# Optimization experiments

Measured on AMD Instinct MI355X. Metric: run time of the kernel, lower is better.

## Reference

```python
import jax, jax.numpy as jnp
import numpy as np

NC = 80
REG_MAX = 16
NO = REG_MAX * 4 + NC  # 144
LEVEL_SHAPES = [(80, 80), (40, 40), (20, 20)]
STRIDES = [8.0, 16.0, 32.0]
CHANNELS = [256, 512, 512]


def _make_anchors():
    """Returns anchor_points (2, A) and stride_tensor (1, A), grid offset 0.5."""
    pts, sts = [], []
    for (h, w), s in zip(LEVEL_SHAPES, STRIDES):
        sx = jnp.arange(w, dtype=jnp.float32) + 0.5
        sy = jnp.arange(h, dtype=jnp.float32) + 0.5
        gy, gx = jnp.meshgrid(sy, sx, indexing='ij')
        pts.append(jnp.stack([gx.ravel(), gy.ravel()], axis=-1))  # (h*w, 2)
        sts.append(jnp.full((h * w,), s, dtype=jnp.float32))
    anchors = jnp.concatenate(pts, axis=0).T          # (2, A)
    strides = jnp.concatenate(sts, axis=0)[None, :]   # (1, A)
    return anchors, strides


def setup_inputs() -> dict:
    key = jax.random.key(0)
    ks = jax.random.split(key, 16)
    inp = {}
    inp['x0'] = jax.random.normal(ks[0], (16, 256, 80, 80), dtype=jnp.float32)
    inp['x1'] = jax.random.normal(ks[1], (16, 512, 40, 40), dtype=jnp.float32)
    inp['x2'] = jax.random.normal(ks[2], (16, 512, 20, 20), dtype=jnp.float32)
    # per-level 1x1 conv head weights: box branch (4*reg_max out), cls branch (nc out)
    for i, c in enumerate(CHANNELS):
        sc = 1.0 / np.sqrt(c)
        inp[f'w_box{i}'] = jax.random.normal(ks[3 + 4 * i], (REG_MAX * 4, c), dtype=jnp.float32) * sc
        inp[f'b_box{i}'] = jax.random.normal(ks[4 + 4 * i], (REG_MAX * 4,), dtype=jnp.float32) * 0.01
        inp[f'w_cls{i}'] = jax.random.normal(ks[5 + 4 * i], (NC, c), dtype=jnp.float32) * sc
        inp[f'b_cls{i}'] = jax.random.normal(ks[6 + 4 * i], (NC,), dtype=jnp.float32) * 0.01
    return inp


def _level_out(x, wb, bb, wc, bc):
    # cat(cv2(x), cv3(x), dim=1) then view(B, no, -1)
    box = jnp.einsum('bchw,oc->bohw', x, wb) + bb[None, :, None, None]
    cls = jnp.einsum('bchw,oc->bohw', x, wc) + bc[None, :, None, None]
    B = x.shape[0]
    return jnp.concatenate([box, cls], axis=1).reshape(B, NO, -1)


def reference(x0, x1, x2,
              w_box0, b_box0, w_cls0, b_cls0,
              w_box1, b_box1, w_cls1, b_cls1,
              w_box2, b_box2, w_cls2, b_cls2):
    xs = [x0, x1, x2]
    wbs = [w_box0, w_box1, w_box2]
    bbs = [b_box0, b_box1, b_box2]
    wcs = [w_cls0, w_cls1, w_cls2]
    bcs = [b_cls0, b_cls1, b_cls2]
    x_cat = jnp.concatenate(
        [_level_out(x, wb, bb, wc, bc) for x, wb, bb, wc, bc in zip(xs, wbs, bbs, wcs, bcs)],
        axis=2)  # (B, 144, A)
    B, _, A = x_cat.shape
    box, cls = x_cat[:, :REG_MAX * 4, :], x_cat[:, REG_MAX * 4:, :]

    # DFL: (B, 4*16, A) -> softmax over 16 bins -> expected distance per side
    p = jax.nn.softmax(box.reshape(B, 4, REG_MAX, A), axis=2)
    dist = jnp.einsum('bkra,r->bka', p, jnp.arange(REG_MAX, dtype=jnp.float32))  # (B, 4, A)

    # dist2bbox (xywh) on anchor grid, scale by stride
    anchors, strides = _make_anchors()
    anc = anchors[None]                 # (1, 2, A)
    lt, rb = dist[:, :2, :], dist[:, 2:, :]
    x1y1 = anc - lt
    x2y2 = anc + rb
    c_xy = (x1y1 + x2y2) * 0.5
    wh = x2y2 - x1y1
    dbox = jnp.concatenate([c_xy, wh], axis=1) * strides[:, None, :]  # (B, 4, A)

    # boxes (B, A, 4), scores (B, A, nc) -- the tensors fed to EfficientNMS_TRT
    boxes = jnp.transpose(dbox, (0, 2, 1))
    scores = jnp.transpose(cls, (0, 2, 1))
    return jnp.concatenate([boxes, scores], axis=-1)  # (B, A, 4 + nc)
```

## Files before the change

kernel.cpp:

```cpp
#include <hip/hip_runtime.h>


typedef __bf16 bf16x8 __attribute__((ext_vector_type(8)));
typedef float  f32x4  __attribute__((ext_vector_type(4)));

#define NTHREADS 256

#define WCHUNK 9216
#define WOFF0 0
#define WOFF1 73728
#define WOFF2 221184

#define XBUF 16384

__device__ __forceinline__ unsigned int pack_bf16(float a, float b) {
    unsigned int ua = __builtin_bit_cast(unsigned int, a);
    unsigned int ub = __builtin_bit_cast(unsigned int, b);
    return ((ua + 0x8000u) >> 16) | ((ub + 0x8000u) & 0xffff0000u);
}

__device__ __forceinline__ int swz32(int row, int kbyte) {
    return row * 64 + (kbyte ^ ((((row & 3) ^ ((row >> 2) & 1))) << 4));
}

__device__ __forceinline__ void gload_lds16(const void* g, void* l) {
    __builtin_amdgcn_global_load_lds(
        (const __attribute__((address_space(1))) void*)g,
        (__attribute__((address_space(3))) void*)l, 16, 0, 0);
}

__global__ __launch_bounds__(256)
void prep_w_kernel(const float* __restrict__ wb0, const float* __restrict__ wc0,
                   const float* __restrict__ wb1, const float* __restrict__ wc1,
                   const float* __restrict__ wb2, const float* __restrict__ wc2,
                   unsigned char* __restrict__ ws) {
    int uid = blockIdx.x * 256 + threadIdx.x;
    if (uid >= 23040) return;
    const float* wb; const float* wc; int C; size_t off; int uu;
    if (uid < 4608)       { wb = wb0; wc = wc0; C = 256; off = WOFF0; uu = uid; }
    else if (uid < 13824) { wb = wb1; wc = wc1; C = 512; off = WOFF1; uu = uid - 4608; }
    else                  { wb = wb2; wc = wc2; C = 512; off = WOFF2; uu = uid - 13824; }
    const int kunits = C / 8;
    const int row = uu / kunits;
    const int k   = (uu % kunits) * 8;
    const float* src = ((row < 64) ? (wb + row * C) : (wc + (row - 64) * C)) + k;
    const float4 f0 = *(const float4*)(src);
    const float4 f1 = *(const float4*)(src + 4);
    uint4 p;
    p.x = pack_bf16(f0.x, f0.y);
    p.y = pack_bf16(f0.z, f0.w);
    p.z = pack_bf16(f1.x, f1.y);
    p.w = pack_bf16(f1.z, f1.w);
    const int chunk = k >> 5;
    const int kg    = (k & 31) >> 3;
    *(uint4*)(ws + off + (size_t)chunk * WCHUNK + swz32(row, kg * 16)) = p;
}

template <int LVL>
__device__ __forceinline__ void run_level(
        int rb,
        const float* __restrict__ x,
        const unsigned char* __restrict__ wimg_all,
        const float* __restrict__ bbox, const float* __restrict__ bcls,
        float* __restrict__ out,
        unsigned char* s_w, unsigned char* s_x) {

    constexpr int    C      = (LVL == 0) ? 256 : 512;
    constexpr int    GW     = (LVL == 0) ? 80 : (LVL == 1 ? 40 : 20);
    constexpr int    HW     = GW * GW;
    constexpr int    AOFF   = (LVL == 0) ? 0 : (LVL == 1 ? 6400 : 8000);
    constexpr float  STRIDE = (LVL == 0) ? 8.0f : (LVL == 1 ? 16.0f : 32.0f);
    constexpr int    TPB    = (HW + 127) / 128;
    constexpr size_t WOFF   = (LVL == 0) ? WOFF0 : (LVL == 1 ? WOFF1 : WOFF2);
    const int nkc = C / 32;

    const int b    = rb / TPB;
    const int tile = rb % TPB;
    int hw0 = tile * 128;
    if (hw0 > HW - 128) hw0 = HW - 128;

    const int tid  = threadIdx.x;
    const int wv   = tid >> 6;
    const int lane = tid & 63;
    const int col  = lane & 15;
    const int q4   = lane >> 4;

    const float* xlev = x + (size_t)b * C * HW;
    const unsigned char* wimg = wimg_all + WOFF;

    const int xg  = (((lane & 31) ^ (wv << 2)) << 2);
    const int xr  = lane >> 5;
    const int xrd0 = (((wv * 32 + col) << 2) ^ (q4 << 6)) + q4 * 8 * 512;
    const int xrd1 = (((wv * 32 + 16 + col) << 2) ^ (q4 << 6)) + q4 * 8 * 512;

    f32x4 acc[9][2];
#pragma unroll
    for (int m = 0; m < 9; ++m) {
        acc[m][0] = (f32x4){0.f, 0.f, 0.f, 0.f};
        acc[m][1] = (f32x4){0.f, 0.f, 0.f, 0.f};
    }

#define XDMA(CC, BUF)                                                       \
    {                                                                       \
        _Pragma("unroll")                                                   \
        for (int _i = 0; _i < 4; ++_i) {                                    \
            const int _r2 = wv * 8 + _i * 2;                                \
            gload_lds16(xlev + (size_t)((CC) * 32 + _r2 + xr) * HW + hw0 + xg, \
                        s_x + (BUF) * XBUF + _r2 * 512);                    \
        }                                                                   \
    }

#define WDMA(CC, BUF)                                                       \
    {                                                                       \
        _Pragma("unroll")                                                   \
        for (int _i = 0; _i < 3; ++_i) {                                    \
            const int _u = tid + _i * 256;                                  \
            if (_u < 576)                                                   \
                gload_lds16(wimg + (size_t)(CC) * WCHUNK + _u * 16,         \
                            s_w + (BUF) * WCHUNK + _u * 16);                \
        }                                                                   \
    }

    XDMA(0, 0);
    WDMA(0, 0);
    __builtin_amdgcn_sched_barrier(0);
    asm volatile("s_waitcnt vmcnt(0)" ::: "memory");
    __builtin_amdgcn_s_barrier();
    __builtin_amdgcn_sched_barrier(0);

    for (int kc = 0; kc < nkc; ++kc) {
        const int cur = kc & 1;
        const bool more = (kc + 1 < nkc);

        if (more) {
            XDMA(kc + 1, cur ^ 1);
            WDMA(kc + 1, cur ^ 1);
        }
        __builtin_amdgcn_sched_barrier(0);

        const unsigned char* xbuf = s_x + cur * XBUF;
        float xf0[8], xf1[8];
#pragma unroll
        for (int j = 0; j < 8; ++j) {
            xf0[j] = *(const float*)(xbuf + xrd0 + j * 512);
            xf1[j] = *(const float*)(xbuf + xrd1 + j * 512);
        }
        uint4 qa, qb;
        qa.x = pack_bf16(xf0[0], xf0[1]); qa.y = pack_bf16(xf0[2], xf0[3]);
        qa.z = pack_bf16(xf0[4], xf0[5]); qa.w = pack_bf16(xf0[6], xf0[7]);
        qb.x = pack_bf16(xf1[0], xf1[1]); qb.y = pack_bf16(xf1[2], xf1[3]);
        qb.z = pack_bf16(xf1[4], xf1[5]); qb.w = pack_bf16(xf1[6], xf1[7]);
        const bf16x8 fA = __builtin_bit_cast(bf16x8, qa);
        const bf16x8 fB = __builtin_bit_cast(bf16x8, qb);

        const unsigned char* wbuf = s_w + cur * WCHUNK;
#pragma unroll
        for (int m = 0; m < 9; ++m) {
            const bf16x8 a_ = *(const bf16x8*)(wbuf + swz32(m * 16 + col, q4 * 16));
            acc[m][0] = __builtin_amdgcn_mfma_f32_16x16x32_bf16(a_, fA, acc[m][0], 0, 0, 0);
            acc[m][1] = __builtin_amdgcn_mfma_f32_16x16x32_bf16(a_, fB, acc[m][1], 0, 0, 0);
        }
        __builtin_amdgcn_sched_barrier(0);

        if (more) {
            asm volatile("s_waitcnt vmcnt(0)" ::: "memory");
            __builtin_amdgcn_s_barrier();
            __builtin_amdgcn_sched_barrier(0);
        }
    }

#undef WDMA
#undef XDMA

    float4 bcv[5];
#pragma unroll
    for (int m = 0; m < 5; ++m)
        bcv[m] = *(const float4*)(bcls + m * 16 + q4 * 4);

    const float LOG2E = 1.44269504088896f;

#pragma unroll
    for (int nf = 0; nf < 2; ++nf) {
        const int alocal = wv * 32 + nf * 16 + col;
        const int hw = hw0 + alocal;

        float dist[4];
#pragma unroll
        for (int g = 0; g < 4; ++g) {
            const float4 bbv = *(const float4*)(bbox + g * 16 + q4 * 4);
            const float v0 = acc[g][nf][0] + bbv.x;
            const float v1 = acc[g][nf][1] + bbv.y;
            const float v2 = acc[g][nf][2] + bbv.z;
            const float v3 = acc[g][nf][3] + bbv.w;
            float mx = fmaxf(fmaxf(v0, v1), fmaxf(v2, v3));
            mx = fmaxf(mx, __shfl_xor(mx, 16));
            mx = fmaxf(mx, __shfl_xor(mx, 32));
            const float e0 = __builtin_amdgcn_exp2f((v0 - mx) * LOG2E);
            const float e1 = __builtin_amdgcn_exp2f((v1 - mx) * LOG2E);
            const float e2 = __builtin_amdgcn_exp2f((v2 - mx) * LOG2E);
            const float e3 = __builtin_amdgcn_exp2f((v3 - mx) * LOG2E);
            float s  = e0 + e1 + e2 + e3;
            float ws = e1 + 2.f * e2 + 3.f * e3 + (float)(q4 * 4) * s;
            s  += __shfl_xor(s, 16);
            s  += __shfl_xor(s, 32);
            ws += __shfl_xor(ws, 16);
            ws += __shfl_xor(ws, 32);
            dist[g] = ws / s;
        }

        const size_t obase = ((size_t)b * 8400 + AOFF + hw) * 84;
        if (q4 == 0) {
            const float ax = (float)(hw % GW) + 0.5f;
            const float ay = (float)(hw / GW) + 0.5f;
            f32x4 bx;
            bx[0] = (ax + 0.5f * (dist[2] - dist[0])) * STRIDE;
            bx[1] = (ay + 0.5f * (dist[3] - dist[1])) * STRIDE;
            bx[2] = (dist[0] + dist[2]) * STRIDE;
            bx[3] = (dist[1] + dist[3]) * STRIDE;
            *(f32x4*)(out + obase) = bx;
        }
#pragma unroll
        for (int m = 0; m < 5; ++m) {
            f32x4 v;
            v[0] = acc[m + 4][nf][0] + bcv[m].x;
            v[1] = acc[m + 4][nf][1] + bcv[m].y;
            v[2] = acc[m + 4][nf][2] + bcv[m].z;
            v[3] = acc[m + 4][nf][3] + bcv[m].w;
            *(f32x4*)(out + obase + 4 + m * 16 + q4 * 4) = v;
        }
    }
}

__global__ __launch_bounds__(NTHREADS, 3)
void UltralyticsDetect_kernel(
        const float* __restrict__ x0, const float* __restrict__ x1, const float* __restrict__ x2,
        const unsigned char* __restrict__ wimg,
        const float* __restrict__ bb0, const float* __restrict__ bc0,
        const float* __restrict__ bb1, const float* __restrict__ bc1,
        const float* __restrict__ bb2, const float* __restrict__ bc2,
        float* __restrict__ out) {

    __shared__ __align__(16) unsigned char s_w[2 * WCHUNK];
    __shared__ __align__(16) unsigned char s_x[2 * XBUF];

    const int bid = blockIdx.x;
    if (bid < 208) {
        run_level<1>(bid, x1, wimg, bb1, bc1, out, s_w, s_x);
    } else if (bid < 272) {
        run_level<2>(bid - 208, x2, wimg, bb2, bc2, out, s_w, s_x);
    } else {
        run_level<0>(bid - 272, x0, wimg, bb0, bc0, out, s_w, s_x);
    }
}

extern "C" void kernel_launch(void* const* d_in, const int* in_sizes, int n_in,
                              void* d_out, int out_size, void* d_ws, size_t ws_size,
                              hipStream_t stream) {
    const float* x0  = (const float*)d_in[0];
    const float* x1  = (const float*)d_in[1];
    const float* x2  = (const float*)d_in[2];
    const float* wb0 = (const float*)d_in[3];
    const float* bb0 = (const float*)d_in[4];
    const float* wc0 = (const float*)d_in[5];
    const float* bc0 = (const float*)d_in[6];
    const float* wb1 = (const float*)d_in[7];
    const float* bb1 = (const float*)d_in[8];
    const float* wc1 = (const float*)d_in[9];
    const float* bc1 = (const float*)d_in[10];
    const float* wb2 = (const float*)d_in[11];
    const float* bb2 = (const float*)d_in[12];
    const float* wc2 = (const float*)d_in[13];
    const float* bc2 = (const float*)d_in[14];

    unsigned char* wimg = (unsigned char*)d_ws;

    prep_w_kernel<<<90, 256, 0, stream>>>(wb0, wc0, wb1, wc1, wb2, wc2, wimg);

    UltralyticsDetect_kernel<<<1072, NTHREADS, 0, stream>>>(
        x0, x1, x2, wimg,
        bb0, bc0, bb1, bc1, bb2, bc2,
        (float*)d_out);
}
```

Measured before the change: 48.30 us.

## Load MFMA weight fragments directly from global memory in lane order, drop LDS weight staging

The weight prep kernel now writes bf16 weights in per-lane MFMA fragment order, so each lane can read its A operand straight from global memory (served from L2/L1) instead of DMA-staging weight chunks into LDS. The weight shared buffer is dropped, which frees LDS and may allow more resident blocks. The per-level template is folded into one kernel with runtime level parameters. The explicit waitcnt and sched barriers are replaced by __syncthreads. The cost is global-load latency on the MFMA operand path inside the inner loop, and weaker scheduling control because the level constants are now runtime values.

```diff
diff --git a/kernel.cpp b/kernel.cpp
--- a/kernel.cpp
+++ b/kernel.cpp
@@ -17,10 +17,6 @@
     unsigned int ua = __builtin_bit_cast(unsigned int, a);
     unsigned int ub = __builtin_bit_cast(unsigned int, b);
     return ((ua + 0x8000u) >> 16) | ((ub + 0x8000u) & 0xffff0000u);
-}
-
-__device__ __forceinline__ int swz32(int row, int kbyte) {
-    return row * 64 + (kbyte ^ ((((row & 3) ^ ((row >> 2) & 1))) << 4));
 }
 
 __device__ __forceinline__ void gload_lds16(const void* g, void* l) {
@@ -51,31 +47,40 @@
     p.y = pack_bf16(f0.z, f0.w);
     p.z = pack_bf16(f1.x, f1.y);
     p.w = pack_bf16(f1.z, f1.w);
-    const int chunk = k >> 5;
-    const int kg    = (k & 31) >> 3;
-    *(uint4*)(ws + off + (size_t)chunk * WCHUNK + swz32(row, kg * 16)) = p;
-}
-
-template <int LVL>
-__device__ __forceinline__ void run_level(
-        int rb,
-        const float* __restrict__ x,
-        const unsigned char* __restrict__ wimg_all,
-        const float* __restrict__ bbox, const float* __restrict__ bcls,
-        float* __restrict__ out,
-        unsigned char* s_w, unsigned char* s_x) {
-
-    constexpr int    C      = (LVL == 0) ? 256 : 512;
-    constexpr int    GW     = (LVL == 0) ? 80 : (LVL == 1 ? 40 : 20);
-    constexpr int    HW     = GW * GW;
-    constexpr int    AOFF   = (LVL == 0) ? 0 : (LVL == 1 ? 6400 : 8000);
-    constexpr float  STRIDE = (LVL == 0) ? 8.0f : (LVL == 1 ? 16.0f : 32.0f);
-    constexpr int    TPB    = (HW + 127) / 128;
-    constexpr size_t WOFF   = (LVL == 0) ? WOFF0 : (LVL == 1 ? WOFF1 : WOFF2);
+    const int kc   = k >> 5;
+    const int m    = row >> 4;
+    const int lane = (row & 15) | (((k & 31) >> 3) << 4);
+    *(uint4*)(ws + off + (size_t)kc * WCHUNK + m * 1024 + lane * 16) = p;
+}
+
+__global__ __launch_bounds__(NTHREADS, 3)
+void UltralyticsDetect_kernel(
+        const float* __restrict__ x0, const float* __restrict__ x1, const float* __restrict__ x2,
+        const unsigned char* __restrict__ wimg,
+        const float* __restrict__ bb0, const float* __restrict__ bc0,
+        const float* __restrict__ bb1, const float* __restrict__ bc1,
+        const float* __restrict__ bb2, const float* __restrict__ bc2,
+        float* __restrict__ out) {
+
+    __shared__ __align__(16) unsigned char s_x[2 * XBUF];
+
+    const int bid = blockIdx.x;
+    const float* x; const float* bbox; const float* bcls;
+    int C, GW, HW, AOFF, TPB, rb; float STRIDE; size_t WOFF;
+    if (bid < 208) {
+        x = x1; bbox = bb1; bcls = bc1; rb = bid;
+        C = 512; GW = 40; HW = 1600; AOFF = 6400; TPB = 13; STRIDE = 16.0f; WOFF = WOFF1;
+    } else if (bid < 272) {
+        x = x2; bbox = bb2; bcls = bc2; rb = bid - 208;
+        C = 512; GW = 20; HW = 400;  AOFF = 8000; TPB = 4;  STRIDE = 32.0f; WOFF = WOFF2;
+    } else {
+        x = x0; bbox = bb0; bcls = bc0; rb = bid - 272;
+        C = 256; GW = 80; HW = 6400; AOFF = 0;    TPB = 50; STRIDE = 8.0f;  WOFF = WOFF0;
+    }
     const int nkc = C / 32;
 
     const int b    = rb / TPB;
-    const int tile = rb % TPB;
+    const int tile = rb - b * TPB;
     int hw0 = tile * 128;
     if (hw0 > HW - 128) hw0 = HW - 128;
 
@@ -86,7 +91,7 @@
     const int q4   = lane >> 4;
 
     const float* xlev = x + (size_t)b * C * HW;
-    const unsigned char* wimg = wimg_all + WOFF;
+    const unsigned char* wlev = wimg + WOFF + (size_t)lane * 16;
 
     const int xg  = (((lane & 31) ^ (wv << 2)) << 2);
     const int xr  = lane >> 5;
@@ -110,35 +115,13 @@
         }                                                                   \
     }
 
-#define WDMA(CC, BUF)                                                       \
-    {                                                                       \
-        _Pragma("unroll")                                                   \
-        for (int _i = 0; _i < 3; ++_i) {                                    \
-            const int _u = tid + _i * 256;                                  \
-            if (_u < 576)                                                   \
-                gload_lds16(wimg + (size_t)(CC) * WCHUNK + _u * 16,         \
-                            s_w + (BUF) * WCHUNK + _u * 16);                \
-        }                                                                   \
-    }
-
     XDMA(0, 0);
-    WDMA(0, 0);
-    __builtin_amdgcn_sched_barrier(0);
-    asm volatile("s_waitcnt vmcnt(0)" ::: "memory");
-    __builtin_amdgcn_s_barrier();
-    __builtin_amdgcn_sched_barrier(0);
+    __syncthreads();
 
     for (int kc = 0; kc < nkc; ++kc) {
-        const int cur = kc & 1;
-        const bool more = (kc + 1 < nkc);
-
-        if (more) {
-            XDMA(kc + 1, cur ^ 1);
-            WDMA(kc + 1, cur ^ 1);
-        }
-        __builtin_amdgcn_sched_barrier(0);
-
-        const unsigned char* xbuf = s_x + cur * XBUF;
+        if (kc + 1 < nkc) XDMA(kc + 1, (kc & 1) ^ 1);
+
+        const unsigned char* xbuf = s_x + (kc & 1) * XBUF;
         float xf0[8], xf1[8];
 #pragma unroll
         for (int j = 0; j < 8; ++j) {
@@ -153,23 +136,17 @@
         const bf16x8 fA = __builtin_bit_cast(bf16x8, qa);
         const bf16x8 fB = __builtin_bit_cast(bf16x8, qb);
 
-        const unsigned char* wbuf = s_w + cur * WCHUNK;
+        const unsigned char* wk = wlev + (size_t)kc * WCHUNK;
 #pragma unroll
         for (int m = 0; m < 9; ++m) {
-            const bf16x8 a_ = *(const bf16x8*)(wbuf + swz32(m * 16 + col, q4 * 16));
+            const bf16x8 a_ = *(const bf16x8*)(wk + m * 1024);
             acc[m][0] = __builtin_amdgcn_mfma_f32_16x16x32_bf16(a_, fA, acc[m][0], 0, 0, 0);
             acc[m][1] = __builtin_amdgcn_mfma_f32_16x16x32_bf16(a_, fB, acc[m][1], 0, 0, 0);
         }
-        __builtin_amdgcn_sched_barrier(0);
-
-        if (more) {
-            asm volatile("s_waitcnt vmcnt(0)" ::: "memory");
-            __builtin_amdgcn_s_barrier();
-            __builtin_amdgcn_sched_barrier(0);
-        }
-    }
-
-#undef WDMA
+
+        __syncthreads();
+    }
+
 #undef XDMA
 
     float4 bcv[5];
@@ -231,28 +208,6 @@
     }
 }
 
-__global__ __launch_bounds__(NTHREADS, 3)
-void UltralyticsDetect_kernel(
-        const float* __restrict__ x0, const float* __restrict__ x1, const float* __restrict__ x2,
-        const unsigned char* __restrict__ wimg,
-        const float* __restrict__ bb0, const float* __restrict__ bc0,
-        const float* __restrict__ bb1, const float* __restrict__ bc1,
-        const float* __restrict__ bb2, const float* __restrict__ bc2,
-        float* __restrict__ out) {
-
-    __shared__ __align__(16) unsigned char s_w[2 * WCHUNK];
-    __shared__ __align__(16) unsigned char s_x[2 * XBUF];
-
-    const int bid = blockIdx.x;
-    if (bid < 208) {
-        run_level<1>(bid, x1, wimg, bb1, bc1, out, s_w, s_x);
-    } else if (bid < 272) {
-        run_level<2>(bid - 208, x2, wimg, bb2, bc2, out, s_w, s_x);
-    } else {
-        run_level<0>(bid - 272, x0, wimg, bb0, bc0, out, s_w, s_x);
-    }
-}
-
 extern "C" void kernel_launch(void* const* d_in, const int* in_sizes, int n_in,
                               void* d_out, int out_size, void* d_ws, size_t ws_size,
                               hipStream_t stream) {
```

Measured after the change: 59.60 us. 1.23x slower.
